# Kernel tuning notes

Measured on AMD Instinct MI355X. Metric: run time of the kernel, lower is better.

Reference implementation:

```python
import jax, jax.numpy as jnp
import numpy as np

N_NODES = 100000
N_EDGES = 1600000
IN_DIM = 3
HID = 128


def setup_inputs() -> dict:
    key = jax.random.key(0)
    ks = jax.random.split(key, 16)
    s = 0.05
    inp = {
        "x": jax.random.normal(ks[0], (N_NODES, IN_DIM), dtype=jnp.float32),
        "pos": jax.random.normal(ks[1], (N_NODES, IN_DIM), dtype=jnp.float32),
        "edge_index": jax.random.randint(ks[2], (2, N_EDGES), 0, N_NODES, dtype=jnp.int64),
        # EdgeConv MLP: Linear(2*IN_DIM, HID) -> ReLU -> Linear(HID, HID)
        "w1": jax.random.normal(ks[3], (2 * IN_DIM, HID), dtype=jnp.float32) * s,
        "b1": jnp.zeros((HID,), dtype=jnp.float32),
        "w2": jax.random.normal(ks[4], (HID, HID), dtype=jnp.float32) * s,
        "b2": jnp.zeros((HID,), dtype=jnp.float32),
        # encoder tail: ReLU -> Linear(HID, HID)
        "w3": jax.random.normal(ks[5], (HID, HID), dtype=jnp.float32) * s,
        "b3": jnp.zeros((HID,), dtype=jnp.float32),
        # decoder: Linear(HID, HID) -> ReLU -> Linear(HID, 3)
        "w4": jax.random.normal(ks[6], (HID, HID), dtype=jnp.float32) * s,
        "b4": jnp.zeros((HID,), dtype=jnp.float32),
        "w5": jax.random.normal(ks[7], (HID, 3), dtype=jnp.float32) * s,
        "b5": jnp.zeros((3,), dtype=jnp.float32),
    }
    return inp


def reference(x, pos, edge_index, w1, b1, w2, b2, w3, b3, w4, b4, w5, b5):
    n = x.shape[0]
    src, dst = edge_index[0], edge_index[1]  # message j(src) -> i(dst)
    xi = x[dst]                               # [E, 3] target features
    xj = x[src]                               # [E, 3] source features
    msg_in = jnp.concatenate([xi, xj - xi], axis=-1)          # [E, 6]
    h = jax.nn.relu(msg_in @ w1 + b1) @ w2 + b2               # [E, HID]
    agg = jax.ops.segment_max(h, dst, num_segments=n)         # [N, HID]
    agg = jnp.where(jnp.isneginf(agg), 0.0, agg)              # nodes with no edges -> 0
    enc = jax.nn.relu(agg) @ w3 + b3                          # [N, HID]
    dec = jax.nn.relu(enc @ w4 + b4) @ w5 + b5                # [N, 3]
    return pos + 0.1 * jnp.tanh(dec)
```

## Files before the change

kernel.cpp:

```cpp
#include <hip/hip_runtime.h>
#include <hip/hip_bf16.h>

typedef __attribute__((ext_vector_type(8))) short short8;
typedef __attribute__((ext_vector_type(4))) float floatx4;
typedef __attribute__((ext_vector_type(2))) unsigned short ushortx2;

#define NHID 128
#define PADROW 136
#define EB 64
#define EB2 128
#define PB 256

__device__ __forceinline__ unsigned short f2bf(float x) {
  unsigned int u = __float_as_uint(x);
  u += 0x7FFFu + ((u >> 16) & 1u);
  return (unsigned short)(u >> 16);
}

__device__ __forceinline__ unsigned int pkbf(float a, float b) {
  __hip_bfloat162 h = __float22bfloat162_rn(make_float2(a, b));
  union { __hip_bfloat162 h; unsigned int u; } cv;
  cv.h = h;
  return cv.u;
}

__device__ __forceinline__ unsigned int pack2(float a, float b) {
  return (unsigned int)f2bf(a) | ((unsigned int)f2bf(b) << 16);
}

__device__ __forceinline__ unsigned int pkmax(unsigned int a, unsigned int b) {
  union { unsigned int u; ushortx2 v; } x, y;
  x.u = a; y.u = b;
  x.v = __builtin_elementwise_max(x.v, y.v);
  return x.u;
}

__device__ __forceinline__ void casmax(unsigned int* ap, unsigned int run) {
  unsigned int old = *ap;
  while (true) {
    unsigned int mx = pkmax(old, run);
    if (mx == old) break;
    unsigned int got = atomicCAS(ap, old, mx);
    if (got == old) break;
    old = got;
  }
}

__device__ __forceinline__ bool detect64(const int* __restrict__ ei) {
  unsigned long long b = __ballot(ei[2 * (threadIdx.x & 63) + 1] != 0);
  return b == 0ULL;
}

__device__ __forceinline__ void load_bfrags(const float* __restrict__ wmat,
                                            short8* bf, int m, int q) {
  #pragma unroll
  for (int kc = 0; kc < 4; ++kc) {
    #pragma unroll
    for (int nt = 0; nt < 8; ++nt) {
      short8 v;
      #pragma unroll
      for (int j = 0; j < 8; ++j)
        v[j] = (short)f2bf(wmat[(kc * 32 + q * 8 + j) * NHID + nt * 16 + m]);
      bf[kc * 8 + nt] = v;
    }
  }
}

__device__ __forceinline__ void load_bfrags_perm(const float* __restrict__ wmat,
                                                 short8* bf, int m, int q) {
  #pragma unroll
  for (int kc = 0; kc < 4; ++kc) {
    #pragma unroll
    for (int nt = 0; nt < 8; ++nt) {
      short8 v;
      #pragma unroll
      for (int j = 0; j < 8; ++j) {
        const int khw = kc * 32 + q * 8 + j;
        const int ctrue = ((khw & 7) << 4) | (khw >> 3);
        v[j] = (short)f2bf(wmat[ctrue * NHID + nt * 16 + m]);
      }
      bf[kc * 8 + nt] = v;
    }
  }
}

__device__ __forceinline__ void mfma_block(const unsigned short* uA,
                                           const short8* bf, floatx4* acc,
                                           int w, int m, int q) {
  #pragma unroll
  for (int kc = 0; kc < 4; ++kc) {
    short8 a = *(const short8*)(uA + (16 * w + m) * PADROW + kc * 32 + q * 8);
    #pragma unroll
    for (int nt = 0; nt < 8; ++nt)
      acc[nt] = __builtin_amdgcn_mfma_f32_16x16x32_bf16(a, bf[kc * 8 + nt],
                                                        acc[nt], 0, 0, 0);
  }
}

__global__ void zero_detect_kernel(float4* __restrict__ p, int n4,
                                   const int* __restrict__ ei, int* __restrict__ flag) {
  if (blockIdx.x == 0 && threadIdx.x < 64) {
    unsigned long long b = __ballot(ei[2 * threadIdx.x + 1] != 0);
    if (threadIdx.x == 0) flag[0] = (b == 0ULL) ? 1 : 0;
  }
  int i = blockIdx.x * blockDim.x + threadIdx.x;
  int stride = gridDim.x * blockDim.x;
  float4 z = make_float4(0.f, 0.f, 0.f, 0.f);
  for (; i < n4; i += stride) p[i] = z;
}


__global__ __launch_bounds__(256) void part_hist(const int* __restrict__ ei,
                                                 int* __restrict__ mat, int E, int nbuck,
                                                 float4* __restrict__ aggz, int n4) {
  const int bl = blockIdx.x, t = threadIdx.x;
  if (bl >= PB) {
    int i = (bl - PB) * 256 + t;
    const int st = (gridDim.x - PB) * 256;
    float4 z = make_float4(0.f, 0.f, 0.f, 0.f);
    for (; i < n4; i += st) aggz[i] = z;
    return;
  }
  __shared__ int hist[512];
  const bool is64 = detect64(ei);
  for (int i = t; i < nbuck; i += 256) hist[i] = 0;
  __syncthreads();
  const int chunk = (E + PB - 1) / PB;
  const int lo = bl * chunk;
  const int hi = min(lo + chunk, E);
  for (int i = lo + t; i < hi; i += 256) {
    int d = is64 ? ei[2 * E + 2 * i] : ei[E + i];
    atomicAdd(&hist[d >> 8], 1);
  }
  __syncthreads();
  for (int bu = t; bu < nbuck; bu += 256) mat[bu * PB + bl] = hist[bu];
}

__global__ __launch_bounds__(256) void scan_rows(int* __restrict__ mat,
                                                 int* __restrict__ btot, int nbuck) {
  __shared__ int sh[256];
  const int bu = blockIdx.x, t = threadIdx.x;
  const int v = mat[bu * PB + t];
  sh[t] = v;
  __syncthreads();
  for (int off = 1; off < 256; off <<= 1) {
    int x = (t >= off) ? sh[t - off] : 0;
    __syncthreads();
    sh[t] += x;
    __syncthreads();
  }
  mat[bu * PB + t] = sh[t] - v;
  if (t == 255) btot[bu] = sh[255];
}

__global__ __launch_bounds__(512) void part_scatter(const int* __restrict__ ei,
                                                    const int* __restrict__ mat,
                                                    const int* __restrict__ btot,
                                                    int* __restrict__ bstart,
                                                    int2* __restrict__ mid, int E, int nbuck) {
  __shared__ int off[512];
  __shared__ int bsS[512];
  const bool is64 = detect64(ei);
  const int bl = blockIdx.x, t = threadIdx.x;
  const int o0 = (t < 256 && t < nbuck) ? btot[t] : 0;
  const int o1 = (t < 256 && t + 256 < nbuck) ? btot[t + 256] : 0;
  if (t < 256) { bsS[t] = o0; bsS[t + 256] = o1; }
  __syncthreads();
  for (int o = 1; o < 256; o <<= 1) {
    int x0 = (t >= o && t < 256) ? bsS[t - o] : 0;
    int x1 = (t >= o && t < 256) ? bsS[256 + t - o] : 0;
    __syncthreads();
    if (t < 256) { bsS[t] += x0; bsS[256 + t] += x1; }
    __syncthreads();
  }
  const int tot0 = bsS[255];
  if (t < 256) bsS[256 + t] += tot0;
  __syncthreads();
  if (t < 256) {
    const int ex0 = bsS[t] - o0;
    const int ex1 = bsS[256 + t] - o1;
    if (bl == 0) { bstart[t] = ex0; bstart[256 + t] = ex1; }
    off[t]       = ex0 + ((t < nbuck) ? mat[t * PB + bl] : 0);
    off[256 + t] = ex1 + ((t + 256 < nbuck) ? mat[(t + 256) * PB + bl] : 0);
  }
  __syncthreads();
  const int chunk = (E + PB - 1) / PB;
  const int lo = bl * chunk;
  const int hi = min(lo + chunk, E);
  for (int i = lo + t; i < hi; i += 512) {
    int s = is64 ? ei[2 * i]         : ei[i];
    int d = is64 ? ei[2 * E + 2 * i] : ei[E + i];
    int p = atomicAdd(&off[d >> 8], 1);
    mid[p] = make_int2(s, d);
  }
}

__global__ __launch_bounds__(512) void bucket_sort(const int2* __restrict__ mid,
                                                   const int* __restrict__ bstart,
                                                   int2* __restrict__ sorted) {
  __shared__ int h[256], cnt[256];
  const int bu = blockIdx.x, t = threadIdx.x;
  const int lo = bstart[bu], hi = bstart[bu + 1];
  if (t < 256) { h[t] = 0; cnt[t] = 0; }
  __syncthreads();
  for (int i = lo + t; i < hi; i += 512) atomicAdd(&h[mid[i].y & 255], 1);
  __syncthreads();
  const int v = (t < 256) ? h[t] : 0;
  for (int off = 1; off < 256; off <<= 1) {
    int x = (t >= off && t < 256) ? h[t - off] : 0;
    __syncthreads();
    if (t < 256) h[t] += x;
    __syncthreads();
  }
  const int excl = (t < 256) ? h[t] - v : 0;
  __syncthreads();
  if (t < 256) h[t] = excl;
  __syncthreads();
  for (int i = lo + t; i < hi; i += 512) {
    int2 e = mid[i];
    const int dl = e.y & 255;
    const int p = lo + h[dl] + atomicAdd(&cnt[dl], 1);
    sorted[p] = e;
  }
}


__global__ __launch_bounds__(512, 2) void edge_sorted_kernel(
    const float* __restrict__ x, const int2* __restrict__ sorted,
    const float* __restrict__ w1, const float* __restrict__ b1,
    const float* __restrict__ w2, const float* __restrict__ b2,
    unsigned int* aggu, int N, int E) {
  __shared__ unsigned short us[EB2 * PADROW];
  __shared__ short8 w2f[2048];
  __shared__ int esS[EB2], edS[EB2];
  __shared__ int pn[2];
  __shared__ unsigned long long maskS[2];
  __shared__ unsigned int pmS[8][64];

  const int t = threadIdx.x;
  const int lane = t & 63;
  const int w = t >> 6;
  const int m = lane & 15;
  const int q = lane >> 4;

  float b1c[8], b2c[8];
  #pragma unroll
  for (int nt = 0; nt < 8; ++nt) { b1c[nt] = b1[nt * 16 + m]; b2c[nt] = b2[nt * 16 + m]; }

  short8 bf1[8];
  #pragma unroll
  for (int nt = 0; nt < 8; ++nt) {
    short8 v;
    #pragma unroll
    for (int j = 0; j < 8; ++j)
      v[j] = (q == 0 && j < 6) ? (short)f2bf(w1[j * NHID + nt * 16 + m]) : (short)0;
    bf1[nt] = v;
  }

  for (int idx = t; idx < 2048; idx += 512) {
    const int fg = idx >> 6, ln = idx & 63;
    const int mm = ln & 15;
    const int kc = fg >> 3, nt = fg & 7;
    short8 v;
    #pragma unroll
    for (int j = 0; j < 8; ++j) {
      const int khw = kc * 32 + (ln >> 4) * 8 + j;
      const int ctrue = ((khw & 7) << 4) | (khw >> 3);
      v[j] = (short)f2bf(w2[ctrue * NHID + nt * 16 + mm]);
    }
    w2f[idx] = v;
  }

  const int jc = t & 63;
  const int quarter = t >> 6;

  const int nbt = (E + EB2 - 1) / EB2;
  __syncthreads();

  int2 sv = make_int2(0, -1);
  {
    const int tile0 = blockIdx.x;
    const int gb = tile0 * EB2;
    if (t < EB2) {
      const int e = gb + t;
      if (tile0 < nbt && e < E) sv = sorted[e];
    } else if (t == EB2) {
      sv.y = (tile0 < nbt && gb > 0) ? sorted[gb - 1].y : -2;
    } else if (t == EB2 + 1) {
      sv.y = (tile0 < nbt && gb + EB2 < E) ? sorted[gb + EB2].y : -2;
    }
  }

  for (int tile = blockIdx.x; tile < nbt; tile += gridDim.x) {
    if (t < EB2) { esS[t] = sv.x; edS[t] = sv.y; }
    else if (t == EB2) pn[0] = sv.y;
    else if (t == EB2 + 1) pn[1] = sv.y;
    __syncthreads();

    if (w == 0) {
      int d0 = edS[lane];
      int dp0 = (lane == 0) ? -9 : edS[lane - 1];
      unsigned long long mk0 = __ballot(lane == 0 || d0 != dp0);
      int d1 = edS[64 + lane];
      int dp1 = edS[63 + lane];
      unsigned long long mk1 = __ballot(d1 != dp1);
      if (lane == 0) { maskS[0] = mk0; maskS[1] = mk1; }
    }

    floatx4 acc[8];
    #pragma unroll
    for (int nt = 0; nt < 8; ++nt) { floatx4 z = {0.f, 0.f, 0.f, 0.f}; acc[nt] = z; }
    short8 a1 = {0, 0, 0, 0, 0, 0, 0, 0};
    if (q == 0) {
      const int e = 16 * w + m;
      const int si = esS[e];
      const int d0 = edS[e];
      const int di = (d0 < 0) ? 0 : d0;
      float xi0 = x[di * 3], xi1 = x[di * 3 + 1], xi2 = x[di * 3 + 2];
      float dd0 = x[si * 3] - xi0, dd1 = x[si * 3 + 1] - xi1, dd2 = x[si * 3 + 2] - xi2;
      union { short8 s; uint4 u; } cv;
      cv.u = make_uint4(pkbf(xi0, xi1), pkbf(xi2, dd0), pkbf(dd1, dd2), 0u);
      a1 = cv.s;
    }
    #pragma unroll
    for (int nt = 0; nt < 8; ++nt)
      acc[nt] = __builtin_amdgcn_mfma_f32_16x16x32_bf16(a1, bf1[nt], acc[nt], 0, 0, 0);

    #pragma unroll
    for (int r = 0; r < 4; ++r) {
      union { short8 s; uint4 u; } cv;
      cv.u = make_uint4(
        pkbf(fmaxf(acc[0][r] + b1c[0], 0.f), fmaxf(acc[1][r] + b1c[1], 0.f)),
        pkbf(fmaxf(acc[2][r] + b1c[2], 0.f), fmaxf(acc[3][r] + b1c[3], 0.f)),
        pkbf(fmaxf(acc[4][r] + b1c[4], 0.f), fmaxf(acc[5][r] + b1c[5], 0.f)),
        pkbf(fmaxf(acc[6][r] + b1c[6], 0.f), fmaxf(acc[7][r] + b1c[7], 0.f)));
      *(short8*)(&us[(16 * w + q * 4 + r) * PADROW + m * 8]) = cv.s;
    }
    __syncthreads();

    #pragma unroll
    for (int nt = 0; nt < 8; ++nt) { floatx4 z = {0.f, 0.f, 0.f, 0.f}; acc[nt] = z; }
    #pragma unroll
    for (int kc = 0; kc < 4; ++kc) {
      short8 a = *(const short8*)(&us[(16 * w + m) * PADROW + kc * 32 + q * 8]);
      #pragma unroll
      for (int nt = 0; nt < 8; ++nt)
        acc[nt] = __builtin_amdgcn_mfma_f32_16x16x32_bf16(a, w2f[(kc * 8 + nt) * 64 + lane],
                                                          acc[nt], 0, 0, 0);
    }
    __syncthreads();

    #pragma unroll
    for (int r = 0; r < 4; ++r) {
      union { short8 s; uint4 u; } cv;
      cv.u = make_uint4(
        pkbf(fmaxf(acc[0][r] + b2c[0], 0.f), fmaxf(acc[1][r] + b2c[1], 0.f)),
        pkbf(fmaxf(acc[2][r] + b2c[2], 0.f), fmaxf(acc[3][r] + b2c[3], 0.f)),
        pkbf(fmaxf(acc[4][r] + b2c[4], 0.f), fmaxf(acc[5][r] + b2c[5], 0.f)),
        pkbf(fmaxf(acc[6][r] + b2c[6], 0.f), fmaxf(acc[7][r] + b2c[7], 0.f)));
      *(short8*)(&us[(16 * w + q * 4 + r) * PADROW + m * 8]) = cv.s;
    }
    __syncthreads();

    {
      const int tn = tile + gridDim.x;
      const int gb = tn * EB2;
      int2 nv = make_int2(0, -1);
      if (t < EB2) {
        const int e = gb + t;
        if (tn < nbt && e < E) nv = sorted[e];
      } else if (t == EB2) {
        nv.y = (tn < nbt && gb > 0) ? sorted[gb - 1].y : -2;
      } else if (t == EB2 + 1) {
        nv.y = (tn < nbt && gb + EB2 < E) ? sorted[gb + EB2].y : -2;
      }
      sv = nv;
    }

    int os = -1, onxt = 0, od = -1; unsigned int opart = 0;
    {
      const unsigned long long mk0 = maskS[0], mk1 = maskS[1];
      const int prevd = pn[0], nextd = pn[1];
      const int r0 = quarter * 16, r1 = r0 + 16;
      const unsigned int* us32 = (const unsigned int*)us;
      int s;
      if (r0 < 64) {
        s = 63 - __builtin_clzll(mk0 & (~0ULL >> (63 - r0)));
      } else {
        unsigned long long hm = mk1 & (~0ULL >> (127 - r0));
        s = hm ? 127 - __builtin_clzll(hm) : 63 - __builtin_clzll(mk0);
      }
      while (s < r1) {
        int nxt;
        if (s < 63) {
          unsigned long long ab = mk0 & (~0ULL << (s + 1));
          if (ab) nxt = __builtin_ffsll((long long)ab) - 1;
          else    nxt = mk1 ? 64 + __builtin_ffsll((long long)mk1) - 1 : 128;
        } else if (s == 63) {
          nxt = mk1 ? 64 + __builtin_ffsll((long long)mk1) - 1 : 128;
        } else if (s < 127) {
          unsigned long long ab = mk1 & (~0ULL << (s - 63));
          nxt = ab ? 64 + __builtin_ffsll((long long)ab) - 1 : 128;
        } else nxt = 128;

        const int lo = (s > r0) ? s : r0;
        const int hi = (nxt < r1) ? nxt : r1;
        unsigned int run = 0;
        for (int r = lo; r < hi; ++r)
          run = pkmax(run, us32[r * (PADROW >> 1) + jc]);

        if (s < r0) {
          pmS[quarter][jc] = run;
        } else if (nxt <= r1) {
          const int d = edS[s];
          if (d >= 0) {
            const bool bnd = (s == 0 && prevd == d) || (nxt == 128 && nextd == d);
            unsigned int* ap = aggu + (size_t)d * 64 + jc;
            if (!bnd) *ap = run;
            else if (run) casmax(ap, run);
          }
        } else {
          os = s; onxt = nxt; od = edS[s]; opart = run;
        }
        s = nxt;
      }
    }
    __syncthreads();

    if (os >= 0 && od >= 0) {
      const int endq = (onxt - 1) >> 4;
      #pragma unroll 4
      for (int qq = quarter + 1; qq <= endq; ++qq)
        opart = pkmax(opart, pmS[qq][jc]);
      const bool bnd = (os == 0 && pn[0] == od) || (onxt == 128 && pn[1] == od);
      unsigned int* ap = aggu + (size_t)od * 64 + jc;
      if (!bnd) *ap = opart;
      else if (opart) casmax(ap, opart);
    }
    __syncthreads();
  }
}


__global__ __launch_bounds__(256, 2) void edge_atomic_kernel(
    const float* __restrict__ x, const int* __restrict__ ei,
    const float* __restrict__ w1, const float* __restrict__ b1,
    const float* __restrict__ w2, const float* __restrict__ b2,
    unsigned int* aggu, const int* __restrict__ flag64, int N, int E) {
  __shared__ unsigned short uA[EB * PADROW];
  __shared__ float w1s[6 * NHID];
  __shared__ float b1s[NHID], b2s[NHID];
  __shared__ int es[EB], ed[EB];

  const int t = threadIdx.x;
  const int lane = t & 63;
  const int w = t >> 6;
  const int m = lane & 15;
  const int q = lane >> 4;

  for (int i = t; i < 6 * NHID; i += 256) w1s[i] = w1[i];
  if (t < NHID) { b1s[t] = b1[t]; b2s[t] = b2[t]; }

  short8 bf[32];
  load_bfrags(w2, bf, m, q);

  const bool is64 = (flag64[0] != 0);
  const int nb = (E + EB - 1) / EB;

  for (int batch = blockIdx.x; batch < nb; batch += gridDim.x) {
    const int gbase = batch * EB;
    if (t < EB) {
      int e = gbase + t;
      es[t] = (e < E) ? (is64 ? ei[2 * e] : ei[e]) : 0;
    } else if (t < 2 * EB) {
      int tt = t - EB;
      int e = gbase + tt;
      ed[tt] = (e < E) ? (is64 ? ei[2 * E + 2 * e] : ei[E + e]) : 0;
    }
    __syncthreads();
    {
      const int e = t >> 2;
      const int c0 = (t & 3) * 32;
      const int si = es[e], di = ed[e];
      float xi0 = x[di * 3], xi1 = x[di * 3 + 1], xi2 = x[di * 3 + 2];
      float msg[6];
      msg[0] = xi0; msg[1] = xi1; msg[2] = xi2;
      msg[3] = x[si * 3] - xi0; msg[4] = x[si * 3 + 1] - xi1; msg[5] = x[si * 3 + 2] - xi2;
      unsigned int* d32 = (unsigned int*)uA;
      const int base32 = (e * PADROW + c0) >> 1;
      #pragma unroll
      for (int cc = 0; cc < 32; cc += 2) {
        float u0 = b1s[c0 + cc], u1 = b1s[c0 + cc + 1];
        #pragma unroll
        for (int d = 0; d < 6; ++d) {
          u0 += msg[d] * w1s[d * NHID + c0 + cc];
          u1 += msg[d] * w1s[d * NHID + c0 + cc + 1];
        }
        d32[base32 + (cc >> 1)] = pack2(fmaxf(u0, 0.f), fmaxf(u1, 0.f));
      }
    }
    __syncthreads();

    floatx4 acc[8];
    #pragma unroll
    for (int nt = 0; nt < 8; ++nt) { floatx4 z = {0.f, 0.f, 0.f, 0.f}; acc[nt] = z; }
    mfma_block(uA, bf, acc, w, m, q);

    #pragma unroll
    for (int nt = 0; nt < 8; ++nt) {
      const int c = nt * 16 + m;
      const float bb = b2s[c];
      const int kst = m * 8 + nt;
      #pragma unroll
      for (int r = 0; r < 4; ++r) {
        const int erow = 16 * w + q * 4 + r;
        if (gbase + erow < E) {
          float hb = acc[nt][r] + bb;
          if (hb > 0.f) {
            unsigned int v = (unsigned int)f2bf(hb);
            casmax(aggu + (size_t)ed[erow] * 64 + (kst >> 1), v << (16 * (kst & 1)));
          }
        }
      }
    }
    __syncthreads();
  }
}


__global__ __launch_bounds__(256, 2) void encdec_kernel(
    const float* __restrict__ w3, const float* __restrict__ b3,
    const float* __restrict__ w4, const float* __restrict__ b4,
    const float* __restrict__ w5, const float* __restrict__ b5,
    const float* __restrict__ pos, const unsigned short* __restrict__ agg16,
    float* __restrict__ out, int N) {
  __shared__ unsigned short uA[EB * PADROW];
  __shared__ short8 w4f[2048];
  __shared__ float w5s[NHID * 3];

  const int t = threadIdx.x;
  const int lane = t & 63;
  const int w = t >> 6;
  const int m = lane & 15;
  const int q = lane >> 4;

  float b3c[8], b4c[8];
  #pragma unroll
  for (int nt = 0; nt < 8; ++nt) { b3c[nt] = b3[nt * 16 + m]; b4c[nt] = b4[nt * 16 + m]; }

  short8 bf3[32];
  load_bfrags_perm(w3, bf3, m, q);

  for (int idx = t; idx < 2048; idx += 256) {
    const int fg = idx >> 6, ln = idx & 63;
    const int mm = ln & 15;
    const int kc = fg >> 3, nt = fg & 7;
    short8 v;
    #pragma unroll
    for (int j = 0; j < 8; ++j) {
      const int khw = kc * 32 + (ln >> 4) * 8 + j;
      const int ctrue = ((khw & 7) << 4) | (khw >> 3);
      v[j] = (short)f2bf(w4[ctrue * NHID + nt * 16 + mm]);
    }
    w4f[idx] = v;
  }
  for (int i = t; i < NHID * 3; i += 256) w5s[i] = w5[i];
  const float b50 = b5[0], b51 = b5[1], b52 = b5[2];

  const int ch = t & 15;
  const int rr = t >> 4;
  const int nb = (N + EB - 1) / EB;
  __syncthreads();

  uint4 rv[4];
  const uint4 uz = make_uint4(0u, 0u, 0u, 0u);
  {
    const int b0 = blockIdx.x;
    #pragma unroll
    for (int k = 0; k < 4; ++k) {
      const int node = b0 * EB + rr + 16 * k;
      rv[k] = (b0 < nb && node < N) ? ((const uint4*)agg16)[(size_t)node * 16 + ch] : uz;
    }
  }

  for (int batch = blockIdx.x; batch < nb; batch += gridDim.x) {
    const int base = batch * EB;
    #pragma unroll
    for (int k = 0; k < 4; ++k)
      *(uint4*)(&uA[(rr + 16 * k) * PADROW + ch * 8]) = rv[k];
    __syncthreads();

    {
      const int nxb = batch + gridDim.x;
      #pragma unroll
      for (int k = 0; k < 4; ++k) {
        const int node = nxb * EB + rr + 16 * k;
        rv[k] = (nxb < nb && node < N) ? ((const uint4*)agg16)[(size_t)node * 16 + ch] : uz;
      }
    }

    floatx4 acc[8];
    #pragma unroll
    for (int nt = 0; nt < 8; ++nt) { floatx4 z = {0.f, 0.f, 0.f, 0.f}; acc[nt] = z; }
    mfma_block(uA, bf3, acc, w, m, q);
    __syncthreads();

    #pragma unroll
    for (int r = 0; r < 4; ++r) {
      union { short8 s; uint4 u; } cv;
      cv.u = make_uint4(
        pkbf(acc[0][r] + b3c[0], acc[1][r] + b3c[1]),
        pkbf(acc[2][r] + b3c[2], acc[3][r] + b3c[3]),
        pkbf(acc[4][r] + b3c[4], acc[5][r] + b3c[5]),
        pkbf(acc[6][r] + b3c[6], acc[7][r] + b3c[7]));
      *(short8*)(&uA[(16 * w + q * 4 + r) * PADROW + m * 8]) = cv.s;
    }
    __syncthreads();

    #pragma unroll
    for (int nt = 0; nt < 8; ++nt) { floatx4 z = {0.f, 0.f, 0.f, 0.f}; acc[nt] = z; }
    #pragma unroll
    for (int kc = 0; kc < 4; ++kc) {
      short8 a = *(const short8*)(&uA[(16 * w + m) * PADROW + kc * 32 + q * 8]);
      #pragma unroll
      for (int nt = 0; nt < 8; ++nt)
        acc[nt] = __builtin_amdgcn_mfma_f32_16x16x32_bf16(a, w4f[(kc * 8 + nt) * 64 + lane],
                                                          acc[nt], 0, 0, 0);
    }

    float p[4][3];
    #pragma unroll
    for (int r = 0; r < 4; ++r) { p[r][0] = 0.f; p[r][1] = 0.f; p[r][2] = 0.f; }
    #pragma unroll
    for (int nt = 0; nt < 8; ++nt) {
      const int c = nt * 16 + m;
      const float bb = b4c[nt];
      const float w50 = w5s[c * 3], w51 = w5s[c * 3 + 1], w52 = w5s[c * 3 + 2];
      #pragma unroll
      for (int r = 0; r < 4; ++r) {
        float tv = fmaxf(acc[nt][r] + bb, 0.f);
        p[r][0] += tv * w50; p[r][1] += tv * w51; p[r][2] += tv * w52;
      }
    }
    #pragma unroll
    for (int off = 8; off >= 1; off >>= 1) {
      #pragma unroll
      for (int r = 0; r < 4; ++r) {
        p[r][0] += __shfl_xor(p[r][0], off, 16);
        p[r][1] += __shfl_xor(p[r][1], off, 16);
        p[r][2] += __shfl_xor(p[r][2], off, 16);
      }
    }
    if (m == 0) {
      #pragma unroll
      for (int r = 0; r < 4; ++r) {
        const int node = base + 16 * w + q * 4 + r;
        if (node < N) {
          out[node * 3]     = pos[node * 3]     + 0.1f * tanhf(p[r][0] + b50);
          out[node * 3 + 1] = pos[node * 3 + 1] + 0.1f * tanhf(p[r][1] + b51);
          out[node * 3 + 2] = pos[node * 3 + 2] + 0.1f * tanhf(p[r][2] + b52);
        }
      }
    }
    __syncthreads();
  }
}

extern "C" void kernel_launch(void* const* d_in, const int* in_sizes, int n_in,
                              void* d_out, int out_size, void* d_ws, size_t ws_size,
                              hipStream_t stream) {
  const float* x   = (const float*)d_in[0];
  const float* pos = (const float*)d_in[1];
  const int*   ei  = (const int*)d_in[2];
  const float* w1  = (const float*)d_in[3];
  const float* b1  = (const float*)d_in[4];
  const float* w2  = (const float*)d_in[5];
  const float* b2  = (const float*)d_in[6];
  const float* w3  = (const float*)d_in[7];
  const float* b3  = (const float*)d_in[8];
  const float* w4  = (const float*)d_in[9];
  const float* b4  = (const float*)d_in[10];
  const float* w5  = (const float*)d_in[11];
  const float* b5  = (const float*)d_in[12];
  float* out = (float*)d_out;

  const int N = in_sizes[0] / 3;
  const int E = in_sizes[2] / 2;
  const int nbuck = (N + 255) >> 8;

  char* ws = (char*)d_ws;
  unsigned short* agg16 = (unsigned short*)ws;
  const size_t aggB = (size_t)N * NHID * sizeof(unsigned short);
  int2* mid    = (int2*)(ws + aggB);
  int2* sorted = (int2*)(ws + aggB + (size_t)E * 8);
  int*  mat    = (int*)(ws + aggB + (size_t)E * 16);
  int*  btot   = mat + (size_t)nbuck * PB;
  int*  bstart = btot + nbuck;
  const size_t needed = aggB + (size_t)E * 16 + ((size_t)nbuck * PB + nbuck + 520) * 4;

  if (ws_size >= needed && nbuck <= 511 && E >= 64) {
    part_hist<<<2048, 256, 0, stream>>>(ei, mat, E, nbuck, (float4*)agg16, N * 16);
    scan_rows<<<nbuck, 256, 0, stream>>>(mat, btot, nbuck);
    part_scatter<<<PB, 512, 0, stream>>>(ei, mat, btot, bstart, mid, E, nbuck);
    bucket_sort<<<nbuck, 512, 0, stream>>>(mid, bstart, sorted);
    edge_sorted_kernel<<<512, 512, 0, stream>>>(x, sorted, w1, b1, w2, b2,
                                                (unsigned int*)agg16, N, E);
  } else {
    int* flag2 = (int*)(ws + aggB);
    zero_detect_kernel<<<2048, 256, 0, stream>>>((float4*)agg16, N * 16, ei, flag2);
    edge_atomic_kernel<<<512, 256, 0, stream>>>(x, ei, w1, b1, w2, b2,
                                                (unsigned int*)agg16, flag2, N, E);
  }
  encdec_kernel<<<512, 256, 0, stream>>>(w3, b3, w4, b4, w5, b5, pos, agg16, out, N);
}
```

Before: 346.7 us.

## Retile second edge GEMM as 2x2 warp grid and scalarize segment metadata

The second MFMA GEMM in the sorted edge kernel is retiled so each warp computes a 32-row by 64-column block instead of 16 rows by 128 columns. Each loaded B fragment is now reused across two row blocks, which cuts LDS traffic for the w2 fragments. Biases are folded into the accumulator initial values, and the mask, boundary and destination values are made wave-uniform with readfirstlane so they live in scalar registers. The trailing barrier at the end of each tile loop is removed, which risks a race on shared buffers if the next iteration's writes overlap with pending reads.

```diff
diff --git a/kernel.cpp b/kernel.cpp
--- a/kernel.cpp
+++ b/kernel.cpp
@@ -242,10 +242,14 @@
   const int w = t >> 6;
   const int m = lane & 15;
   const int q = lane >> 4;
-
-  float b1c[8], b2c[8];
+  const int rowg = w >> 1;
+  const int colg = w & 1;
+
+  float b1c[8], b2c[4];
   #pragma unroll
-  for (int nt = 0; nt < 8; ++nt) { b1c[nt] = b1[nt * 16 + m]; b2c[nt] = b2[nt * 16 + m]; }
+  for (int nt = 0; nt < 8; ++nt) b1c[nt] = b1[nt * 16 + m];
+  #pragma unroll
+  for (int nt = 0; nt < 4; ++nt) b2c[nt] = b2[(4 * colg + nt) * 16 + m];
 
   short8 bf1[8];
   #pragma unroll
@@ -309,7 +313,10 @@
 
     floatx4 acc[8];
     #pragma unroll
-    for (int nt = 0; nt < 8; ++nt) { floatx4 z = {0.f, 0.f, 0.f, 0.f}; acc[nt] = z; }
+    for (int nt = 0; nt < 8; ++nt) {
+      floatx4 bz = {b1c[nt], b1c[nt], b1c[nt], b1c[nt]};
+      acc[nt] = bz;
+    }
     short8 a1 = {0, 0, 0, 0, 0, 0, 0, 0};
     if (q == 0) {
       const int e = 16 * w + m;
@@ -330,35 +337,47 @@
     for (int r = 0; r < 4; ++r) {
       union { short8 s; uint4 u; } cv;
       cv.u = make_uint4(
-        pkbf(fmaxf(acc[0][r] + b1c[0], 0.f), fmaxf(acc[1][r] + b1c[1], 0.f)),
-        pkbf(fmaxf(acc[2][r] + b1c[2], 0.f), fmaxf(acc[3][r] + b1c[3], 0.f)),
-        pkbf(fmaxf(acc[4][r] + b1c[4], 0.f), fmaxf(acc[5][r] + b1c[5], 0.f)),
-        pkbf(fmaxf(acc[6][r] + b1c[6], 0.f), fmaxf(acc[7][r] + b1c[7], 0.f)));
+        pkbf(fmaxf(acc[0][r], 0.f), fmaxf(acc[1][r], 0.f)),
+        pkbf(fmaxf(acc[2][r], 0.f), fmaxf(acc[3][r], 0.f)),
+        pkbf(fmaxf(acc[4][r], 0.f), fmaxf(acc[5][r], 0.f)),
+        pkbf(fmaxf(acc[6][r], 0.f), fmaxf(acc[7][r], 0.f)));
       *(short8*)(&us[(16 * w + q * 4 + r) * PADROW + m * 8]) = cv.s;
     }
     __syncthreads();
 
     #pragma unroll
-    for (int nt = 0; nt < 8; ++nt) { floatx4 z = {0.f, 0.f, 0.f, 0.f}; acc[nt] = z; }
+    for (int rb = 0; rb < 2; ++rb)
+      #pragma unroll
+      for (int nt = 0; nt < 4; ++nt) {
+        floatx4 bz = {b2c[nt], b2c[nt], b2c[nt], b2c[nt]};
+        acc[rb * 4 + nt] = bz;
+      }
     #pragma unroll
     for (int kc = 0; kc < 4; ++kc) {
-      short8 a = *(const short8*)(&us[(16 * w + m) * PADROW + kc * 32 + q * 8]);
-      #pragma unroll
-      for (int nt = 0; nt < 8; ++nt)
-        acc[nt] = __builtin_amdgcn_mfma_f32_16x16x32_bf16(a, w2f[(kc * 8 + nt) * 64 + lane],
-                                                          acc[nt], 0, 0, 0);
-    }
-    __syncthreads();
-
-    #pragma unroll
-    for (int r = 0; r < 4; ++r) {
-      union { short8 s; uint4 u; } cv;
-      cv.u = make_uint4(
-        pkbf(fmaxf(acc[0][r] + b2c[0], 0.f), fmaxf(acc[1][r] + b2c[1], 0.f)),
-        pkbf(fmaxf(acc[2][r] + b2c[2], 0.f), fmaxf(acc[3][r] + b2c[3], 0.f)),
-        pkbf(fmaxf(acc[4][r] + b2c[4], 0.f), fmaxf(acc[5][r] + b2c[5], 0.f)),
-        pkbf(fmaxf(acc[6][r] + b2c[6], 0.f), fmaxf(acc[7][r] + b2c[7], 0.f)));
-      *(short8*)(&us[(16 * w + q * 4 + r) * PADROW + m * 8]) = cv.s;
+      short8 bB[4];
+      #pragma unroll
+      for (int nt = 0; nt < 4; ++nt)
+        bB[nt] = w2f[(kc * 8 + 4 * colg + nt) * 64 + lane];
+      #pragma unroll
+      for (int rb = 0; rb < 2; ++rb) {
+        short8 a = *(const short8*)(&us[(32 * rowg + 16 * rb + m) * PADROW + kc * 32 + q * 8]);
+        #pragma unroll
+        for (int nt = 0; nt < 4; ++nt)
+          acc[rb * 4 + nt] = __builtin_amdgcn_mfma_f32_16x16x32_bf16(a, bB[nt],
+                                                                     acc[rb * 4 + nt], 0, 0, 0);
+      }
+    }
+    __syncthreads();
+
+    #pragma unroll
+    for (int rb = 0; rb < 2; ++rb) {
+      #pragma unroll
+      for (int r = 0; r < 4; ++r) {
+        uint2 uu;
+        uu.x = pkbf(fmaxf(acc[rb * 4 + 0][r], 0.f), fmaxf(acc[rb * 4 + 1][r], 0.f));
+        uu.y = pkbf(fmaxf(acc[rb * 4 + 2][r], 0.f), fmaxf(acc[rb * 4 + 3][r], 0.f));
+        *(uint2*)(&us[(32 * rowg + 16 * rb + q * 4 + r) * PADROW + m * 8 + 4 * colg]) = uu;
+      }
     }
     __syncthreads();
 
@@ -378,9 +397,17 @@
     }
 
     int os = -1, onxt = 0, od = -1; unsigned int opart = 0;
+    int prevd, nextd;
     {
-      const unsigned long long mk0 = maskS[0], mk1 = maskS[1];
-      const int prevd = pn[0], nextd = pn[1];
+      const unsigned long long t0 = maskS[0], t1 = maskS[1];
+      const unsigned long long mk0 =
+          (((unsigned long long)(unsigned int)__builtin_amdgcn_readfirstlane((int)(t0 >> 32))) << 32) |
+          (unsigned long long)(unsigned int)__builtin_amdgcn_readfirstlane((int)(t0 & 0xffffffffu));
+      const unsigned long long mk1 =
+          (((unsigned long long)(unsigned int)__builtin_amdgcn_readfirstlane((int)(t1 >> 32))) << 32) |
+          (unsigned long long)(unsigned int)__builtin_amdgcn_readfirstlane((int)(t1 & 0xffffffffu));
+      prevd = __builtin_amdgcn_readfirstlane(pn[0]);
+      nextd = __builtin_amdgcn_readfirstlane(pn[1]);
       const int r0 = quarter * 16, r1 = r0 + 16;
       const unsigned int* us32 = (const unsigned int*)us;
       int s;
@@ -412,7 +439,7 @@
         if (s < r0) {
           pmS[quarter][jc] = run;
         } else if (nxt <= r1) {
-          const int d = edS[s];
+          const int d = __builtin_amdgcn_readfirstlane(edS[s]);
           if (d >= 0) {
             const bool bnd = (s == 0 && prevd == d) || (nxt == 128 && nextd == d);
             unsigned int* ap = aggu + (size_t)d * 64 + jc;
@@ -420,7 +447,9 @@
             else if (run) casmax(ap, run);
           }
         } else {
-          os = s; onxt = nxt; od = edS[s]; opart = run;
+          os = s; onxt = nxt;
+          od = __builtin_amdgcn_readfirstlane(edS[s]);
+          opart = run;
         }
         s = nxt;
       }
@@ -432,12 +461,11 @@
       #pragma unroll 4
       for (int qq = quarter + 1; qq <= endq; ++qq)
         opart = pkmax(opart, pmS[qq][jc]);
-      const bool bnd = (os == 0 && pn[0] == od) || (onxt == 128 && pn[1] == od);
+      const bool bnd = (os == 0 && prevd == od) || (onxt == 128 && nextd == od);
       unsigned int* ap = aggu + (size_t)od * 64 + jc;
       if (!bnd) *ap = opart;
       else if (opart) casmax(ap, opart);
     }
-    __syncthreads();
   }
 }
 
```

After: 416.8 us. 1.2x slower.
